# Kernel tuning notes

Hardware: AMD Instinct MI355X
Metric: run time of the kernel (lower is better)

The kernel has to match this reference:

```python
import jax, jax.numpy as jnp
import numpy as np
import math

NUM_HEADS = 16

def setup_inputs() -> dict:
    key = jax.random.key(0)
    k1, k2, k3 = jax.random.split(key, 3)
    B, L, C = 4, 2048, 1024
    # xavier-uniform-ish scale for weights
    input = jax.random.normal(k1, (B, L, C), dtype=jnp.float32)
    w_in = jax.random.uniform(k2, (3 * C, C), dtype=jnp.float32, minval=-1.0, maxval=1.0) * math.sqrt(6.0 / (4 * C))
    w_out = jax.random.uniform(k3, (C, C), dtype=jnp.float32, minval=-1.0, maxval=1.0) * math.sqrt(6.0 / (2 * C))
    return {"input": input, "w_in": w_in, "w_out": w_out}

def reference(input, w_in, w_out):
    B, L, C = input.shape
    H = NUM_HEADS
    D = C // H
    qkv = input @ w_in.T                      # [B, L, 3C]
    q, k, v = jnp.split(qkv, 3, axis=-1)
    # [B, H, L, D]
    q = q.reshape(B, L, H, D).transpose(0, 2, 1, 3)
    k = k.reshape(B, L, H, D).transpose(0, 2, 1, 3)
    v = v.reshape(B, L, H, D).transpose(0, 2, 1, 3)
    scale = 1.0 / math.sqrt(D)
    scores = scale * jnp.einsum('bhqd,bhkd->bhqk', q, k)  # [B, H, L, L]
    causal = jnp.tril(jnp.ones((L, L), dtype=bool))
    scores = jnp.where(causal, scores, -jnp.inf)
    attn = jax.nn.softmax(scores, axis=-1)
    ctx = jnp.einsum('bhqk,bhkd->bhqd', attn, v)          # [B, H, L, D]
    ctx = ctx.transpose(0, 2, 1, 3).reshape(B, L, C)
    return ctx @ w_out.T
```

## Files before the change

kernel.cpp:

```cpp
#include <hip/hip_runtime.h>
#include <math.h>

typedef __bf16 bf16_t;
typedef __attribute__((ext_vector_type(8))) __bf16 bf16x8;
typedef __attribute__((ext_vector_type(4))) float f32x4;
typedef __attribute__((ext_vector_type(16))) float f32x16;

#define AS_G __attribute__((address_space(1)))
#define AS_L __attribute__((address_space(3)))

__device__ __forceinline__ f32x4 mfma16(bf16x8 a, bf16x8 b, f32x4 c) {
  return __builtin_amdgcn_mfma_f32_16x16x32_bf16(a, b, c, 0, 0, 0);
}
__device__ __forceinline__ f32x16 mfma32(bf16x8 a, bf16x8 b, f32x16 c) {
  return __builtin_amdgcn_mfma_f32_32x32x16_bf16(a, b, c, 0, 0, 0);
}

__device__ __forceinline__ void gload16(const bf16_t* g, bf16_t* l) {
  __builtin_amdgcn_global_load_lds((const AS_G void*)g, (AS_L void*)l, 16, 0, 0);
}

__global__ void cvt_f32_bf16_k(const float* __restrict__ in, bf16_t* __restrict__ out, int n4) {
  int i = blockIdx.x * blockDim.x + threadIdx.x;
  int stride = gridDim.x * blockDim.x;
  for (; i < n4; i += stride) {
    float4 v = reinterpret_cast<const float4*>(in)[i];
    union { bf16_t b[4]; short4 s; } u;
    u.b[0] = (bf16_t)v.x; u.b[1] = (bf16_t)v.y;
    u.b[2] = (bf16_t)v.z; u.b[3] = (bf16_t)v.w;
    reinterpret_cast<short4*>(out)[i] = u.s;
  }
}

template <int EPI>
__global__ __launch_bounds__(256)
void gemm_bt(const bf16_t* __restrict__ A, const bf16_t* __restrict__ Bm,
             bf16_t* __restrict__ q_out, bf16_t* __restrict__ k_out,
             bf16_t* __restrict__ vt_out, float* __restrict__ f_out,
             int M, int N, int K) {
  __shared__ __align__(16) bf16_t lA[128 * 32];
  __shared__ __align__(16) bf16_t lB[128 * 32];
  const int lane = threadIdx.x & 63;
  const int wid = threadIdx.x >> 6;
  const int m0 = blockIdx.y * 128;
  const int n0 = blockIdx.x * 128;
  const int wr = (wid >> 1) * 64;
  const int wc = (wid & 1) * 64;
  const int lr = lane & 15;
  const int lg = lane >> 4;
  const int srow = lane >> 2;
  const int scol = (lane & 3) * 8;
  const int s0 = wid * 2, s1 = s0 + 1;

  f32x4 acc[4][4] = {};

  for (int k0 = 0; k0 < K; k0 += 32) {
    gload16(A + (size_t)(m0 + s0 * 16 + srow) * K + k0 + scol, &lA[s0 * 512]);
    gload16(A + (size_t)(m0 + s1 * 16 + srow) * K + k0 + scol, &lA[s1 * 512]);
    gload16(Bm + (size_t)(n0 + s0 * 16 + srow) * K + k0 + scol, &lB[s0 * 512]);
    gload16(Bm + (size_t)(n0 + s1 * 16 + srow) * K + k0 + scol, &lB[s1 * 512]);
    __syncthreads();
    bf16x8 af[4], bfr[4];
#pragma unroll
    for (int m = 0; m < 4; ++m)
      af[m] = *reinterpret_cast<const bf16x8*>(&lA[(wr + m * 16 + lr) * 32 + lg * 8]);
#pragma unroll
    for (int n = 0; n < 4; ++n)
      bfr[n] = *reinterpret_cast<const bf16x8*>(&lB[(wc + n * 16 + lr) * 32 + lg * 8]);
#pragma unroll
    for (int m = 0; m < 4; ++m)
#pragma unroll
      for (int n = 0; n < 4; ++n)
        acc[m][n] = mfma16(af[m], bfr[n], acc[m][n]);
    __syncthreads();
  }

  if (EPI == 0) {
#pragma unroll
    for (int n = 0; n < 4; ++n) {
      const int gn = n0 + wc + n * 16 + lr;
      const int sec = gn >> 10;
      const int hd = gn & 1023;
      const int h = hd >> 6, d = hd & 63;
#pragma unroll
      for (int m = 0; m < 4; ++m) {
        const int gm0 = m0 + wr + m * 16 + lg * 4;
        if (sec == 0) {
#pragma unroll
          for (int r = 0; r < 4; ++r) {
            const int gm = gm0 + r;
            q_out[((size_t)((gm >> 11) * 16 + h) * 2048 + (gm & 2047)) * 64 + d] =
                (bf16_t)(acc[m][n][r] * 0.125f);
          }
        } else if (sec == 1) {
#pragma unroll
          for (int r = 0; r < 4; ++r) {
            const int gm = gm0 + r;
            k_out[((size_t)((gm >> 11) * 16 + h) * 2048 + (gm & 2047)) * 64 + d] =
                (bf16_t)acc[m][n][r];
          }
        } else {
          union { bf16_t b[4]; short4 s; } u;
#pragma unroll
          for (int r = 0; r < 4; ++r) u.b[r] = (bf16_t)acc[m][n][r];
          const int b = gm0 >> 11, sl = gm0 & 2047;
          *reinterpret_cast<short4*>(
              &vt_out[((size_t)(b * 16 + h) * 64 + d) * 2048 + sl]) = u.s;
        }
      }
    }
  } else {
#pragma unroll
    for (int m = 0; m < 4; ++m) {
      const int gm0 = m0 + wr + m * 16 + lg * 4;
#pragma unroll
      for (int n = 0; n < 4; ++n) {
        const int gn = n0 + wc + n * 16 + lr;
#pragma unroll
        for (int r = 0; r < 4; ++r)
          f_out[(size_t)(gm0 + r) * N + gn] = acc[m][n][r];
      }
    }
  }
}

__global__ __launch_bounds__(256)
void attn_fwd(const bf16_t* __restrict__ Q, const bf16_t* __restrict__ Km,
              const bf16_t* __restrict__ Vt, bf16_t* __restrict__ ctx, int L) {
  __shared__ __align__(16) bf16_t lK[2][64 * 64];
  __shared__ __align__(16) bf16_t lV[2][64 * 64];

  const int lane = threadIdx.x & 63;
  const int wid = threadIdx.x >> 6;
  const int nid = (blockIdx.x & 7) * 128 + (blockIdx.x >> 3);
  const int bh = nid >> 4;
  const int qt = 15 - (nid & 15);
  const int q32 = lane & 31;
  const int hi = lane >> 5;
  const int q0w = qt * 128 + wid * 32;
  const int qrow = q0w + q32;
  const bf16_t* Qh = Q + (size_t)bh * L * 64;
  const bf16_t* Kh = Km + (size_t)bh * L * 64;
  const bf16_t* Vh = Vt + (size_t)bh * 64 * L;

  bf16x8 bq[4];
#pragma unroll
  for (int c = 0; c < 4; ++c)
    bq[c] = *reinterpret_cast<const bf16x8*>(&Qh[(size_t)qrow * 64 + c * 16 + hi * 8]);

  f32x16 oacc[2] = {};
  float m_run = -1e30f, l_run = 0.f;

  const int sr0 = wid * 8 + (lane >> 3);
  const int sc = ((lane & 7) ^ (sr0 & 7)) * 8;
  const int nt = 2 * qt + 2;

#define STAGE(buf, kb)                                                      \
  do {                                                                      \
    gload16(Kh + (size_t)((kb) + sr0) * 64 + sc, &lK[buf][wid * 512]);      \
    gload16(Kh + (size_t)((kb) + sr0 + 32) * 64 + sc,                       \
            &lK[buf][2048 + wid * 512]);                                    \
    gload16(Vh + (size_t)sr0 * L + (kb) + sc, &lV[buf][wid * 512]);         \
    gload16(Vh + (size_t)(sr0 + 32) * L + (kb) + sc,                        \
            &lV[buf][2048 + wid * 512]);                                    \
  } while (0)

  STAGE(0, 0);
  int cur = 0;
  for (int t = 0; t < nt; ++t) {
    __syncthreads();
    if (t + 1 < nt) STAGE(cur ^ 1, (t + 1) * 64);
    const int kb = t * 64;
    if (kb <= q0w + 31) {
      const bf16_t* tK = lK[cur];
      const bf16_t* tV = lV[cur];
      f32x16 sacc[2] = {};
#pragma unroll
      for (int n = 0; n < 2; ++n) {
        const int row = n * 32 + q32;
        const int rx = row & 7;
#pragma unroll
        for (int c = 0; c < 4; ++c) {
          bf16x8 ak = *reinterpret_cast<const bf16x8*>(
              &tK[row * 64 + ((2 * c + hi) ^ rx) * 8]);
          sacc[n] = mfma32(ak, bq[c], sacc[n]);
        }
      }
      if (kb + 63 > q0w) {
#pragma unroll
        for (int n = 0; n < 2; ++n)
#pragma unroll
          for (int r = 0; r < 16; ++r) {
            const int kg = kb + n * 32 + (r & 3) + 4 * hi + 8 * (r >> 2);
            if (kg > qrow) sacc[n][r] = -1e30f;
          }
      }
      float v8[8];
#pragma unroll
      for (int i = 0; i < 8; ++i)
        v8[i] = fmaxf(fmaxf(sacc[0][i], sacc[0][i + 8]),
                      fmaxf(sacc[1][i], sacc[1][i + 8]));
      float v4a = fmaxf(v8[0], v8[4]), v4b = fmaxf(v8[1], v8[5]);
      float v4c = fmaxf(v8[2], v8[6]), v4d = fmaxf(v8[3], v8[7]);
      float pm = fmaxf(fmaxf(v4a, v4b), fmaxf(v4c, v4d));
      pm = fmaxf(pm, __shfl_xor(pm, 32));
      if (__any(pm > m_run + 8.f)) {
        const float mn = fmaxf(m_run, pm);
        const float al = __expf(m_run - mn);
#pragma unroll
        for (int ms = 0; ms < 2; ++ms)
#pragma unroll
          for (int r = 0; r < 16; ++r) oacc[ms][r] *= al;
        l_run *= al;
        m_run = mn;
      }
      float ls = 0.f;
#pragma unroll
      for (int n = 0; n < 2; ++n)
#pragma unroll
        for (int r = 0; r < 16; ++r) {
          const float p = __expf(sacc[n][r] - m_run);
          sacc[n][r] = p;
          ls += p;
        }
      ls += __shfl_xor(ls, 32);
      l_run += ls;
      bf16x8 pb[4];
#pragma unroll
      for (int n = 0; n < 2; ++n) {
        int w[8], pw[8];
#pragma unroll
        for (int j = 0; j < 8; ++j) {
          union { bf16_t b[2]; int i; } u;
          u.b[0] = (bf16_t)sacc[n][2 * j];
          u.b[1] = (bf16_t)sacc[n][2 * j + 1];
          w[j] = u.i;
        }
#pragma unroll
        for (int j = 0; j < 8; ++j) pw[j] = __shfl_xor(w[j], 32);
#pragma unroll
        for (int s = 0; s < 2; ++s) {
          union { int i[4]; bf16x8 v; } pv;
          if (hi == 0) {
            pv.i[0] = w[4 * s];     pv.i[1] = w[4 * s + 1];
            pv.i[2] = pw[4 * s];    pv.i[3] = pw[4 * s + 1];
          } else {
            pv.i[0] = pw[4 * s + 2]; pv.i[1] = pw[4 * s + 3];
            pv.i[2] = w[4 * s + 2];  pv.i[3] = w[4 * s + 3];
          }
          pb[2 * n + s] = pv.v;
        }
      }
#pragma unroll
      for (int s4 = 0; s4 < 4; ++s4) {
#pragma unroll
        for (int ms = 0; ms < 2; ++ms) {
          const int row = ms * 32 + q32;
          bf16x8 av = *reinterpret_cast<const bf16x8*>(
              &tV[row * 64 + ((2 * s4 + hi) ^ (row & 7)) * 8]);
          oacc[ms] = mfma32(av, pb[s4], oacc[ms]);
        }
      }
    }
    cur ^= 1;
  }
#undef STAGE
  const float inv = 1.f / l_run;
  const int b = bh >> 4, h = bh & 15;
  const size_t orow = (size_t)(b * 2048 + qrow) * 1024 + h * 64;
#pragma unroll
  for (int ms = 0; ms < 2; ++ms)
#pragma unroll
    for (int rg = 0; rg < 4; ++rg) {
      union { bf16_t b4[4]; short4 s; } u;
#pragma unroll
      for (int i = 0; i < 4; ++i) u.b4[i] = (bf16_t)(oacc[ms][rg * 4 + i] * inv);
      *reinterpret_cast<short4*>(&ctx[orow + ms * 32 + rg * 8 + hi * 4]) = u.s;
    }
}

extern "C" void kernel_launch(void* const* d_in, const int* in_sizes, int n_in,
                              void* d_out, int out_size, void* d_ws, size_t ws_size,
                              hipStream_t stream) {
  (void)in_sizes; (void)n_in; (void)out_size; (void)ws_size;
  const float* x     = (const float*)d_in[0];
  const float* w_in  = (const float*)d_in[1];
  const float* w_out = (const float*)d_in[2];
  float* out = (float*)d_out;

  char* ws = (char*)d_ws;
  bf16_t* xb   = (bf16_t*)(ws);
  bf16_t* wib  = (bf16_t*)(ws + 16777216);
  bf16_t* wob  = (bf16_t*)(ws + 23068672);
  bf16_t* Qb   = (bf16_t*)(ws + 25165824);
  bf16_t* Kb   = (bf16_t*)(ws + 41943040);
  bf16_t* Vtb  = (bf16_t*)(ws + 58720256);
  bf16_t* ctxb = (bf16_t*)(ws + 75497472);

  const int M = 8192, C = 1024, L = 2048;

  {
    int n4 = 8388608 / 4, blk = (n4 + 255) / 256; if (blk > 2048) blk = 2048;
    cvt_f32_bf16_k<<<blk, 256, 0, stream>>>(x, xb, n4);
  }
  {
    int n4 = 3145728 / 4, blk = (n4 + 255) / 256; if (blk > 2048) blk = 2048;
    cvt_f32_bf16_k<<<blk, 256, 0, stream>>>(w_in, wib, n4);
  }
  {
    int n4 = 1048576 / 4, blk = (n4 + 255) / 256; if (blk > 2048) blk = 2048;
    cvt_f32_bf16_k<<<blk, 256, 0, stream>>>(w_out, wob, n4);
  }

  gemm_bt<0><<<dim3(3072 / 128, M / 128), 256, 0, stream>>>(
      xb, wib, Qb, Kb, Vtb, nullptr, M, 3072, C);

  attn_fwd<<<1024, 256, 0, stream>>>(Qb, Kb, Vtb, ctxb, L);

  gemm_bt<1><<<dim3(C / 128, M / 128), 256, 0, stream>>>(
      ctxb, wob, nullptr, nullptr, nullptr, out, M, C, C);
}
```

Baseline: 305.0 us.

## Pair long and short causal query tiles per attention block for load balance

Each attention block now processes two 128-row query tiles of the same head, tile 15-p and tile p, so every block does the same amount of causal work. K/V tiles staged once in LDS are shared by both query tiles, which halves the grid to 512 blocks. The goal is to remove the tail imbalance of the causal triangle and reuse K/V loads. In exchange it doubles the accumulator register state per thread, which may lower occupancy, and leaves fewer blocks to spread across CUs.

Result: faster. 282.4 us (-7.4%).

```diff
diff --git a/kernel.cpp b/kernel.cpp
--- a/kernel.cpp
+++ b/kernel.cpp
@@ -124,6 +124,115 @@
   }
 }
 
+__device__ __forceinline__ void attn_tile(
+    const bf16_t* __restrict__ tK, const bf16_t* __restrict__ tV,
+    int kb, int q0w, int qrow, int q32, int hi,
+    const bf16x8 bq[4], f32x16 oacc[2], float& m_run, float& l_run) {
+  f32x16 sacc[2] = {};
+#pragma unroll
+  for (int n = 0; n < 2; ++n) {
+    const int row = n * 32 + q32;
+    const int rx = row & 7;
+#pragma unroll
+    for (int c = 0; c < 4; ++c) {
+      bf16x8 ak = *reinterpret_cast<const bf16x8*>(
+          &tK[row * 64 + ((2 * c + hi) ^ rx) * 8]);
+      sacc[n] = mfma32(ak, bq[c], sacc[n]);
+    }
+  }
+  if (kb + 63 > q0w) {
+#pragma unroll
+    for (int n = 0; n < 2; ++n)
+#pragma unroll
+      for (int r = 0; r < 16; ++r) {
+        const int kg = kb + n * 32 + (r & 3) + 4 * hi + 8 * (r >> 2);
+        if (kg > qrow) sacc[n][r] = -1e30f;
+      }
+  }
+  float v8[8];
+#pragma unroll
+  for (int i = 0; i < 8; ++i)
+    v8[i] = fmaxf(fmaxf(sacc[0][i], sacc[0][i + 8]),
+                  fmaxf(sacc[1][i], sacc[1][i + 8]));
+  float pm = fmaxf(fmaxf(fmaxf(v8[0], v8[4]), fmaxf(v8[1], v8[5])),
+                   fmaxf(fmaxf(v8[2], v8[6]), fmaxf(v8[3], v8[7])));
+  pm = fmaxf(pm, __shfl_xor(pm, 32));
+  if (__any(pm > m_run + 8.f)) {
+    const float mn = fmaxf(m_run, pm);
+    const float al = __expf(m_run - mn);
+#pragma unroll
+    for (int ms = 0; ms < 2; ++ms)
+#pragma unroll
+      for (int r = 0; r < 16; ++r) oacc[ms][r] *= al;
+    l_run *= al;
+    m_run = mn;
+  }
+  float ls = 0.f;
+#pragma unroll
+  for (int n = 0; n < 2; ++n)
+#pragma unroll
+    for (int r = 0; r < 16; ++r) {
+      const float p = __expf(sacc[n][r] - m_run);
+      sacc[n][r] = p;
+      ls += p;
+    }
+  ls += __shfl_xor(ls, 32);
+  l_run += ls;
+  bf16x8 pb[4];
+#pragma unroll
+  for (int n = 0; n < 2; ++n) {
+    int w[8], pw[8];
+#pragma unroll
+    for (int j = 0; j < 8; ++j) {
+      union { bf16_t b[2]; int i; } u;
+      u.b[0] = (bf16_t)sacc[n][2 * j];
+      u.b[1] = (bf16_t)sacc[n][2 * j + 1];
+      w[j] = u.i;
+    }
+#pragma unroll
+    for (int j = 0; j < 8; ++j) pw[j] = __shfl_xor(w[j], 32);
+#pragma unroll
+    for (int s = 0; s < 2; ++s) {
+      union { int i[4]; bf16x8 v; } pv;
+      if (hi == 0) {
+        pv.i[0] = w[4 * s];      pv.i[1] = w[4 * s + 1];
+        pv.i[2] = pw[4 * s];     pv.i[3] = pw[4 * s + 1];
+      } else {
+        pv.i[0] = pw[4 * s + 2]; pv.i[1] = pw[4 * s + 3];
+        pv.i[2] = w[4 * s + 2];  pv.i[3] = w[4 * s + 3];
+      }
+      pb[2 * n + s] = pv.v;
+    }
+  }
+#pragma unroll
+  for (int s4 = 0; s4 < 4; ++s4) {
+#pragma unroll
+    for (int ms = 0; ms < 2; ++ms) {
+      const int row = ms * 32 + q32;
+      bf16x8 av = *reinterpret_cast<const bf16x8*>(
+          &tV[row * 64 + ((2 * s4 + hi) ^ (row & 7)) * 8]);
+      oacc[ms] = mfma32(av, pb[s4], oacc[ms]);
+    }
+  }
+}
+
+__device__ __forceinline__ void attn_epi(bf16_t* __restrict__ ctx, int bh,
+                                         int qrow, int hi,
+                                         const f32x16 oacc[2], float l_run) {
+  const float inv = 1.f / l_run;
+  const int b = bh >> 4, h = bh & 15;
+  const size_t orow = (size_t)(b * 2048 + qrow) * 1024 + h * 64;
+#pragma unroll
+  for (int ms = 0; ms < 2; ++ms)
+#pragma unroll
+    for (int rg = 0; rg < 4; ++rg) {
+      union { bf16_t b4[4]; short4 s; } u;
+#pragma unroll
+      for (int i = 0; i < 4; ++i) u.b4[i] = (bf16_t)(oacc[ms][rg * 4 + i] * inv);
+      *reinterpret_cast<short4*>(&ctx[orow + ms * 32 + rg * 8 + hi * 4]) = u.s;
+    }
+}
+
 __global__ __launch_bounds__(256)
 void attn_fwd(const bf16_t* __restrict__ Q, const bf16_t* __restrict__ Km,
               const bf16_t* __restrict__ Vt, bf16_t* __restrict__ ctx, int L) {
@@ -132,28 +241,31 @@
 
   const int lane = threadIdx.x & 63;
   const int wid = threadIdx.x >> 6;
-  const int nid = (blockIdx.x & 7) * 128 + (blockIdx.x >> 3);
-  const int bh = nid >> 4;
-  const int qt = 15 - (nid & 15);
+  const int nid = (blockIdx.x & 7) * 64 + (blockIdx.x >> 3);
+  const int bh = nid >> 3;
+  const int p = nid & 7;
+  const int jA = 15 - p, jB = p;
   const int q32 = lane & 31;
   const int hi = lane >> 5;
-  const int q0w = qt * 128 + wid * 32;
-  const int qrow = q0w + q32;
+  const int q0A = jA * 128 + wid * 32, qrowA = q0A + q32;
+  const int q0B = jB * 128 + wid * 32, qrowB = q0B + q32;
   const bf16_t* Qh = Q + (size_t)bh * L * 64;
   const bf16_t* Kh = Km + (size_t)bh * L * 64;
   const bf16_t* Vh = Vt + (size_t)bh * 64 * L;
 
-  bf16x8 bq[4];
-#pragma unroll
-  for (int c = 0; c < 4; ++c)
-    bq[c] = *reinterpret_cast<const bf16x8*>(&Qh[(size_t)qrow * 64 + c * 16 + hi * 8]);
-
-  f32x16 oacc[2] = {};
-  float m_run = -1e30f, l_run = 0.f;
+  bf16x8 bqA[4], bqB[4];
+#pragma unroll
+  for (int c = 0; c < 4; ++c) {
+    bqA[c] = *reinterpret_cast<const bf16x8*>(&Qh[(size_t)qrowA * 64 + c * 16 + hi * 8]);
+    bqB[c] = *reinterpret_cast<const bf16x8*>(&Qh[(size_t)qrowB * 64 + c * 16 + hi * 8]);
+  }
+
+  f32x16 oaccA[2] = {}, oaccB[2] = {};
+  float mA = -1e30f, lA_ = 0.f, mB = -1e30f, lB_ = 0.f;
 
   const int sr0 = wid * 8 + (lane >> 3);
   const int sc = ((lane & 7) ^ (sr0 & 7)) * 8;
-  const int nt = 2 * qt + 2;
+  const int nt = 2 * jA + 2;
 
 #define STAGE(buf, kb)                                                      \
   do {                                                                      \
@@ -171,112 +283,17 @@
     __syncthreads();
     if (t + 1 < nt) STAGE(cur ^ 1, (t + 1) * 64);
     const int kb = t * 64;
-    if (kb <= q0w + 31) {
-      const bf16_t* tK = lK[cur];
-      const bf16_t* tV = lV[cur];
-      f32x16 sacc[2] = {};
-#pragma unroll
-      for (int n = 0; n < 2; ++n) {
-        const int row = n * 32 + q32;
-        const int rx = row & 7;
-#pragma unroll
-        for (int c = 0; c < 4; ++c) {
-          bf16x8 ak = *reinterpret_cast<const bf16x8*>(
-              &tK[row * 64 + ((2 * c + hi) ^ rx) * 8]);
-          sacc[n] = mfma32(ak, bq[c], sacc[n]);
-        }
-      }
-      if (kb + 63 > q0w) {
-#pragma unroll
-        for (int n = 0; n < 2; ++n)
-#pragma unroll
-          for (int r = 0; r < 16; ++r) {
-            const int kg = kb + n * 32 + (r & 3) + 4 * hi + 8 * (r >> 2);
-            if (kg > qrow) sacc[n][r] = -1e30f;
-          }
-      }
-      float v8[8];
-#pragma unroll
-      for (int i = 0; i < 8; ++i)
-        v8[i] = fmaxf(fmaxf(sacc[0][i], sacc[0][i + 8]),
-                      fmaxf(sacc[1][i], sacc[1][i + 8]));
-      float v4a = fmaxf(v8[0], v8[4]), v4b = fmaxf(v8[1], v8[5]);
-      float v4c = fmaxf(v8[2], v8[6]), v4d = fmaxf(v8[3], v8[7]);
-      float pm = fmaxf(fmaxf(v4a, v4b), fmaxf(v4c, v4d));
-      pm = fmaxf(pm, __shfl_xor(pm, 32));
-      if (__any(pm > m_run + 8.f)) {
-        const float mn = fmaxf(m_run, pm);
-        const float al = __expf(m_run - mn);
-#pragma unroll
-        for (int ms = 0; ms < 2; ++ms)
-#pragma unroll
-          for (int r = 0; r < 16; ++r) oacc[ms][r] *= al;
-        l_run *= al;
-        m_run = mn;
-      }
-      float ls = 0.f;
-#pragma unroll
-      for (int n = 0; n < 2; ++n)
-#pragma unroll
-        for (int r = 0; r < 16; ++r) {
-          const float p = __expf(sacc[n][r] - m_run);
-          sacc[n][r] = p;
-          ls += p;
-        }
-      ls += __shfl_xor(ls, 32);
-      l_run += ls;
-      bf16x8 pb[4];
-#pragma unroll
-      for (int n = 0; n < 2; ++n) {
-        int w[8], pw[8];
-#pragma unroll
-        for (int j = 0; j < 8; ++j) {
-          union { bf16_t b[2]; int i; } u;
-          u.b[0] = (bf16_t)sacc[n][2 * j];
-          u.b[1] = (bf16_t)sacc[n][2 * j + 1];
-          w[j] = u.i;
-        }
-#pragma unroll
-        for (int j = 0; j < 8; ++j) pw[j] = __shfl_xor(w[j], 32);
-#pragma unroll
-        for (int s = 0; s < 2; ++s) {
-          union { int i[4]; bf16x8 v; } pv;
-          if (hi == 0) {
-            pv.i[0] = w[4 * s];     pv.i[1] = w[4 * s + 1];
-            pv.i[2] = pw[4 * s];    pv.i[3] = pw[4 * s + 1];
-          } else {
-            pv.i[0] = pw[4 * s + 2]; pv.i[1] = pw[4 * s + 3];
-            pv.i[2] = w[4 * s + 2];  pv.i[3] = w[4 * s + 3];
-          }
-          pb[2 * n + s] = pv.v;
-        }
-      }
-#pragma unroll
-      for (int s4 = 0; s4 < 4; ++s4) {
-#pragma unroll
-        for (int ms = 0; ms < 2; ++ms) {
-          const int row = ms * 32 + q32;
-          bf16x8 av = *reinterpret_cast<const bf16x8*>(
-              &tV[row * 64 + ((2 * s4 + hi) ^ (row & 7)) * 8]);
-          oacc[ms] = mfma32(av, pb[s4], oacc[ms]);
-        }
-      }
-    }
+    const bf16_t* tK = lK[cur];
+    const bf16_t* tV = lV[cur];
+    if (kb <= q0A + 31)
+      attn_tile(tK, tV, kb, q0A, qrowA, q32, hi, bqA, oaccA, mA, lA_);
+    if (kb <= q0B + 31)
+      attn_tile(tK, tV, kb, q0B, qrowB, q32, hi, bqB, oaccB, mB, lB_);
     cur ^= 1;
   }
 #undef STAGE
-  const float inv = 1.f / l_run;
-  const int b = bh >> 4, h = bh & 15;
-  const size_t orow = (size_t)(b * 2048 + qrow) * 1024 + h * 64;
-#pragma unroll
-  for (int ms = 0; ms < 2; ++ms)
-#pragma unroll
-    for (int rg = 0; rg < 4; ++rg) {
-      union { bf16_t b4[4]; short4 s; } u;
-#pragma unroll
-      for (int i = 0; i < 4; ++i) u.b4[i] = (bf16_t)(oacc[ms][rg * 4 + i] * inv);
-      *reinterpret_cast<short4*>(&ctx[orow + ms * 32 + rg * 8 + hi * 4]) = u.s;
-    }
+  attn_epi(ctx, bh, qrowA, hi, oaccA, lA_);
+  attn_epi(ctx, bh, qrowB, hi, oaccB, lB_);
 }
 
 extern "C" void kernel_launch(void* const* d_in, const int* in_sizes, int n_in,
@@ -315,7 +332,7 @@
   gemm_bt<0><<<dim3(3072 / 128, M / 128), 256, 0, stream>>>(
       xb, wib, Qb, Kb, Vtb, nullptr, M, 3072, C);
 
-  attn_fwd<<<1024, 256, 0, stream>>>(Qb, Kb, Vtb, ctxb, L);
+  attn_fwd<<<512, 256, 0, stream>>>(Qb, Kb, Vtb, ctxb, L);
 
   gemm_bt<1><<<dim3(C / 128, M / 128), 256, 0, stream>>>(
       ctxb, wob, nullptr, nullptr, nullptr, out, M, C, C);
```
